# Performance work log

Measured on AMD Instinct MI355X. Metric: run time of the kernel, lower is better.

## Reference

```python
import jax, jax.numpy as jnp
import numpy as np

SCALE_POS = 2.0
SCALE_NEG = 50.0
THRESH = 0.7
MARGIN = 0.1
GAMMA = 0.3
EPS = 1e-5       # epsilon excluding self / near-duplicate positives
COS_EPS = 1e-8   # torch CosineSimilarity eps


def setup_inputs() -> dict:
    key = jax.random.key(0)
    k1, k2 = jax.random.split(key)
    B, D, C = 4096, 128, 256
    emb = jax.random.normal(k1, (B, D), dtype=jnp.float32)
    emb = emb / jnp.linalg.norm(emb, axis=1, keepdims=True)  # metric-learning embeddings are L2-normalized
    labels = jax.random.randint(k2, (B,), 0, C)
    return {"embeddings": emb, "labels": labels}


def reference(embeddings, labels):
    B = embeddings.shape[0]
    sim = embeddings @ embeddings.T                                   # [B,B]
    same = labels[:, None] == labels[None, :]
    pos_mask = same & (sim < 1.0 - EPS)
    neg_mask = ~same
    inf = jnp.inf
    min_pos = jnp.min(jnp.where(pos_mask, sim, inf), axis=1)          # [B] min(pos_pair_)
    max_neg = jnp.max(jnp.where(neg_mask, sim, -inf), axis=1)         # [B] max(neg_pair_)
    neg_keep = neg_mask & (sim + MARGIN > min_pos[:, None])           # mined negatives
    pos_keep = pos_mask & (sim - MARGIN < max_neg[:, None])           # mined positives
    valid = jnp.any(neg_keep, axis=1) & jnp.any(pos_keep, axis=1)
    # hardest positive index per anchor (argmin over kept positives; first-min tie-break like torch)
    j = jnp.argmin(jnp.where(pos_keep, sim, inf), axis=1)             # [B]
    d_p = embeddings[j] - embeddings                                  # f_p - f_a, [B,D]
    # dot[i,n] = (e_n - e_i) . d_p[i]
    dot = jnp.einsum('nd,id->in', embeddings, d_p) \
        - jnp.einsum('id,id->i', embeddings, d_p)[:, None]            # [B,B]
    sq = jnp.sum(embeddings * embeddings, axis=1)                     # [B]
    # ||e_n - e_i|| via Gram matrix; clamp avoids inf grad of sqrt at the diagonal (masked anyway)
    norm_n = jnp.sqrt(jnp.maximum(sq[None, :] + sq[:, None] - 2.0 * sim, 1e-12))
    norm_p = jnp.linalg.norm(d_p, axis=1)                             # [B] ||f_p - f_a||
    denom = jnp.maximum(norm_n, COS_EPS) * jnp.maximum(norm_p, COS_EPS)[:, None]
    reg = GAMMA * dot / denom                                         # [B,B] gamma * cos(f_n-f_a, f_p-f_a)
    pos_terms = jnp.where(pos_keep, jnp.exp(-SCALE_POS * (sim - THRESH)), 0.0)
    neg_terms = jnp.where(neg_keep, jnp.exp(SCALE_NEG * (sim - THRESH - reg)), 0.0)
    pos_loss = jnp.log1p(jnp.sum(pos_terms, axis=1)) / SCALE_POS
    neg_loss = jnp.log1p(jnp.sum(neg_terms, axis=1)) / SCALE_NEG
    row_loss = jnp.where(valid, pos_loss + neg_loss, 0.0)
    return jnp.sum(row_loss) / B
```

## Files before the change

### kernel.cpp

```cpp
#include <hip/hip_runtime.h>
#include <math.h>

#define NB 4096

#define SCALE_POS 2.0f
#define SCALE_NEG 50.0f
#define THRESH    0.7f
#define MARGIN    0.1f
#define GAMMA     0.3f
#define EPS_SELF  1e-5f

typedef __attribute__((ext_vector_type(8))) short s16x8;
typedef __attribute__((ext_vector_type(16))) float f32x16;
typedef unsigned long long u64;
typedef unsigned int u32;
typedef unsigned char u8;

__device__ __forceinline__ short f2bf(float x) {
  u32 u = __float_as_uint(x);
  return (short)((u + 0x7FFFu + ((u >> 16) & 1u)) >> 16);
}
__device__ __forceinline__ float bf2f(short h) {
  return __uint_as_float(((u32)(unsigned short)h) << 16);
}
__device__ __forceinline__ u32 mono16(u32 h) {
  return (h & 0x8000u) ? (h ^ 0xFFFFu) : (h | 0x8000u);
}
__device__ __forceinline__ float unmono16(u32 m) {
  u32 h = (m & 0x8000u) ? (m & 0x7FFFu) : (~m & 0xFFFFu);
  return bf2f((short)h);
}
__device__ __forceinline__ int Lmap(int p) {
  return (p & ~63) + 2 * (p & 31) + ((p >> 5) & 1);
}
__device__ __forceinline__ int Linv(int c) {
  return (c & ~63) + ((c & 1) << 5) + ((c >> 1) & 31);
}

__global__ __launch_bounds__(256) void k1_convert(
    const float* __restrict__ emb, const int* __restrict__ labels,
    short* __restrict__ F, u8* __restrict__ labu8) {
  int t = blockIdx.x * 256 + threadIdx.x;
  int T = t >> 9, s = (t >> 6) & 7, l = t & 63;
  int lrow = Lmap(T * 32 + (l & 31));
  int c4 = s * 4 + (l >> 5) * 2;
  const float4* e4 = (const float4*)emb;
  float4 v0 = e4[lrow * 32 + c4];
  float4 v1 = e4[lrow * 32 + c4 + 1];
  float xs[8] = {v0.x, v0.y, v0.z, v0.w, v1.x, v1.y, v1.z, v1.w};
  s16x8 h, lo;
#pragma unroll
  for (int e = 0; e < 8; ++e) {
    short hh = f2bf(xs[e]);
    h[e] = hh;
    lo[e] = f2bf(xs[e] - bf2f(hh));
  }
  ((s16x8*)F)[(T * 16 + s) * 64 + l] = h;
  ((s16x8*)F)[(T * 16 + 8 + s) * 64 + l] = lo;
  if (t < 1024) {
    int4 lb = ((const int4*)labels)[t];
    uchar4 p;
    p.x = (u8)lb.x; p.y = (u8)lb.y; p.z = (u8)lb.z; p.w = (u8)lb.w;
    ((uchar4*)labu8)[t] = p;
  }
}

__global__ __launch_bounds__(256, 4) void k2_pass1(
    const short* __restrict__ F, short* __restrict__ simh) {
  int tid = threadIdx.x, w = tid >> 6, l = tid & 63;
  int lo5 = l & 31, hi = l >> 5;
  int mt0 = blockIdx.y * 4 + (w >> 1) * 2;
  int nt0 = blockIdx.x * 4 + (w & 1) * 2;
  const s16x8* F8 = (const s16x8*)F;

  f32x16 acc[2][2] = {};
#pragma unroll 1
  for (int s = 0; s < 8; ++s) {
    s16x8 ah[2], al[2], bh[2], bl[2];
#pragma unroll
    for (int t = 0; t < 2; ++t) {
      int ia = ((mt0 + t) * 16 + s) * 64 + l;
      int ib = ((nt0 + t) * 16 + s) * 64 + l;
      ah[t] = F8[ia]; al[t] = F8[ia + 512];
      bh[t] = F8[ib]; bl[t] = F8[ib + 512];
    }
#pragma unroll
    for (int ti = 0; ti < 2; ++ti)
#pragma unroll
      for (int tj = 0; tj < 2; ++tj) {
        acc[ti][tj] = __builtin_amdgcn_mfma_f32_32x32x16_bf16(ah[ti], bh[tj], acc[ti][tj], 0, 0, 0);
        acc[ti][tj] = __builtin_amdgcn_mfma_f32_32x32x16_bf16(ah[ti], bl[tj], acc[ti][tj], 0, 0, 0);
        acc[ti][tj] = __builtin_amdgcn_mfma_f32_32x32x16_bf16(al[ti], bh[tj], acc[ti][tj], 0, 0, 0);
      }
  }

  u32* sim32 = (u32*)simh;
  int cg = nt0 >> 1;
#pragma unroll
  for (int ti = 0; ti < 2; ++ti)
#pragma unroll
    for (int q = 0; q < 4; ++q)
#pragma unroll
      for (int rr = 0; rr < 4; ++rr) {
        int reg = q * 4 + rr;
        int m = (mt0 + ti) * 32 + q * 8 + hi * 4 + rr;
        u32 pv = ((u32)(unsigned short)f2bf(acc[ti][1][reg]) << 16) |
                 (u32)(unsigned short)f2bf(acc[ti][0][reg]);
        sim32[(size_t)m * (NB / 2) + cg * 32 + lo5] = pv;
      }
}

__global__ __launch_bounds__(256) void k4_row(
    const short* __restrict__ simh, const u8* __restrict__ labu8,
    float* __restrict__ rowloss) {
  int w = threadIdx.x >> 6, l = threadIdx.x & 63;
  int r = w >> 1;
  int h = w & 1;
  int i = blockIdx.x * 2 + r;
  int lm = (int)labu8[Lmap(i)];
  const s16x8* sI = (const s16x8*)(simh + (size_t)i * NB);
  const u64* L8 = (const u64*)labu8;
  int cbase = h * 256;

  s16x8 a[4];
  u64 lab[4];
#pragma unroll
  for (int ch = 0; ch < 4; ++ch) a[ch] = sI[cbase + ch * 64 + l];
#pragma unroll
  for (int ch = 0; ch < 4; ++ch) lab[ch] = L8[cbase + ch * 64 + l];

  u32 pk = 0xFFFFFFFFu;
  u32 nk = 0u;
  u32 posm = 0u;
#pragma unroll
  for (int ch = 0; ch < 4; ++ch) {
    int nb = (cbase + ch * 64 + l) * 8;
#pragma unroll
    for (int e = 0; e < 8; ++e) {
      u32 hb = (u32)(unsigned short)a[ch][e];
      u32 key = (mono16(hb) << 16) | (u32)(nb + e);
      int ln = (int)((lab[ch] >> (8 * e)) & 255u);
      if (ln == lm) {
        posm |= (1u << (ch * 8 + e));
        float s = bf2f((short)hb);
        if (s < 1.0f - EPS_SELF) pk = pk < key ? pk : key;
      } else {
        nk = nk > key ? nk : key;
      }
    }
  }
#pragma unroll
  for (int d = 1; d < 64; d <<= 1) {
    u32 po = __shfl_xor(pk, d, 64); pk = pk < po ? pk : po;
    u32 no = __shfl_xor(nk, d, 64); nk = nk > no ? nk : no;
  }
  __shared__ u32 spk[4], snk[4];
  if (l == 0) { spk[w] = pk; snk[w] = nk; }
  __syncthreads();
  u32 P0 = spk[r * 2], P1 = spk[r * 2 + 1];
  u32 N0 = snk[r * 2], N1 = snk[r * 2 + 1];
  u32 Pk = P0 < P1 ? P0 : P1;
  u32 Nk = N0 > N1 ? N0 : N1;
  float minpos = unmono16(Pk >> 16);
  float maxneg = unmono16(Nk >> 16);
  bool valid = (maxneg + MARGIN > minpos);
  int jp = valid ? Linv((int)(Pk & 0xFFFFu)) : i;
  float mp = minpos, mx = maxneg;
  float dpp = minpos - 1.0f;
  float inpp = rsqrtf(fmaxf(2.0f - 2.0f * minpos, 1e-12f));

  const s16x8* sJ = (const s16x8*)(simh + (size_t)jp * NB);
  s16x8 b[4];
#pragma unroll
  for (int ch = 0; ch < 4; ++ch) b[ch] = sJ[cbase + ch * 64 + l];

  float ps = 0.0f, ns = 0.0f;
#pragma unroll
  for (int ch = 0; ch < 4; ++ch) {
#pragma unroll
    for (int e = 0; e < 8; ++e) {
      float s = bf2f(a[ch][e]);
      if ((posm >> (ch * 8 + e)) & 1u) {
        if (s < 1.0f - EPS_SELF && s - MARGIN < mx)
          ps += __expf(-SCALE_POS * (s - THRESH));
      } else if (s + MARGIN > mp) {
        float sjv = bf2f(b[ch][e]);
        float inn = rsqrtf(fmaxf(2.0f - 2.0f * s, 1e-12f));
        float rg = GAMMA * (sjv - s - dpp) * inpp * inn;
        ns += __expf(SCALE_NEG * (s - THRESH - rg));
      }
    }
  }
#pragma unroll
  for (int d = 1; d < 64; d <<= 1) {
    ps += __shfl_xor(ps, d, 64);
    ns += __shfl_xor(ns, d, 64);
  }
  __shared__ float redp[4], redn[4];
  if (l == 0) { redp[w] = ps; redn[w] = ns; }
  __syncthreads();
  if (l == 0 && h == 0) {
    float tp = redp[r * 2] + redp[r * 2 + 1];
    float tn = redn[r * 2] + redn[r * 2 + 1];
    rowloss[i] = valid ? (log1pf(tp) * (1.0f / SCALE_POS) + log1pf(tn) * (1.0f / SCALE_NEG))
                       : 0.0f;
  }
}

__global__ __launch_bounds__(1024) void k5_final(
    const float* __restrict__ rowloss, float* __restrict__ out) {
  int tid = threadIdx.x;
  float local = 0.0f;
  for (int r = tid; r < NB; r += 1024) local += rowloss[r];
#pragma unroll
  for (int d = 1; d < 64; d <<= 1) local += __shfl_xor(local, d, 64);
  __shared__ float partial[16];
  if ((tid & 63) == 0) partial[tid >> 6] = local;
  __syncthreads();
  if (tid == 0) {
    float t = 0.0f;
#pragma unroll
    for (int q = 0; q < 16; ++q) t += partial[q];
    out[0] = t / (float)NB;
  }
}

extern "C" void kernel_launch(void* const* d_in, const int* in_sizes, int n_in,
                              void* d_out, int out_size, void* d_ws, size_t ws_size,
                              hipStream_t stream) {
  const float* emb = (const float*)d_in[0];
  const int* labels = (const int*)d_in[1];
  float* out = (float*)d_out;
  char* ws = (char*)d_ws;

  short* simh = (short*)ws;
  short* F = (short*)(ws + ((size_t)NB * NB * 2));
  char* base = ws + ((size_t)NB * NB * 2) + (2 << 20);
  float* rowloss = (float*)(base);
  u8* labu8 = (u8*)(base + 16384);

  hipLaunchKernelGGL(k1_convert, dim3(256), dim3(256), 0, stream,
                     emb, labels, F, labu8);
  hipLaunchKernelGGL(k2_pass1, dim3(NB / 128, NB / 128), dim3(256), 0, stream,
                     F, simh);
  hipLaunchKernelGGL(k4_row, dim3(NB / 2), dim3(256), 0, stream,
                     simh, labu8, rowloss);
  hipLaunchKernelGGL(k5_final, dim3(1), dim3(1024), 0, stream, rowloss, out);
}
```

Before: 52.61 us.

## Fuse min-positive/max-negative mining into GEMM epilogue with atomic keys

Moves the per-row hardest-positive and hardest-negative key reduction from the row kernel into the GEMM epilogue. Each thread reduces packed (similarity, index) keys over its tile's column slice and merges them with global atomicMin/atomicMax, relying on the similarity matrix being symmetric. The init kernel resets the key arrays. This removes the row kernel's first reduction phase (shuffles, shared-memory sync and mask building), at the cost of extra label loads, compares and atomics in the GEMM epilogue.

```diff
diff --git a/kernel.cpp b/kernel.cpp
--- a/kernel.cpp
+++ b/kernel.cpp
@@ -33,13 +33,11 @@
 __device__ __forceinline__ int Lmap(int p) {
   return (p & ~63) + 2 * (p & 31) + ((p >> 5) & 1);
 }
-__device__ __forceinline__ int Linv(int c) {
-  return (c & ~63) + ((c & 1) << 5) + ((c >> 1) & 31);
-}
 
 __global__ __launch_bounds__(256) void k1_convert(
     const float* __restrict__ emb, const int* __restrict__ labels,
-    short* __restrict__ F, u8* __restrict__ labu8) {
+    short* __restrict__ F, u8* __restrict__ labu8,
+    u32* __restrict__ minkey, u32* __restrict__ maxkey) {
   int t = blockIdx.x * 256 + threadIdx.x;
   int T = t >> 9, s = (t >> 6) & 7, l = t & 63;
   int lrow = Lmap(T * 32 + (l & 31));
@@ -63,10 +61,16 @@
     p.x = (u8)lb.x; p.y = (u8)lb.y; p.z = (u8)lb.z; p.w = (u8)lb.w;
     ((uchar4*)labu8)[t] = p;
   }
+  if (t < NB) {
+    minkey[t] = 0xFFFFFFFFu;
+    maxkey[t] = 0u;
+  }
 }
 
 __global__ __launch_bounds__(256, 4) void k2_pass1(
-    const short* __restrict__ F, short* __restrict__ simh) {
+    const short* __restrict__ F, const u8* __restrict__ labu8,
+    short* __restrict__ simh,
+    u32* __restrict__ minkey, u32* __restrict__ maxkey) {
   int tid = threadIdx.x, w = tid >> 6, l = tid & 63;
   int lo5 = l & 31, hi = l >> 5;
   int mt0 = blockIdx.y * 4 + (w >> 1) * 2;
@@ -96,6 +100,11 @@
 
   u32* sim32 = (u32*)simh;
   int cg = nt0 >> 1;
+  int c0 = cg * 64 + 2 * lo5;
+  int lmc0 = (int)labu8[c0], lmc1 = (int)labu8[c0 + 1];
+  u32 mn0 = 0xFFFFFFFFu, mn1 = 0xFFFFFFFFu;
+  u32 mx0 = 0u, mx1 = 0u;
+
 #pragma unroll
   for (int ti = 0; ti < 2; ++ti)
 #pragma unroll
@@ -104,75 +113,63 @@
       for (int rr = 0; rr < 4; ++rr) {
         int reg = q * 4 + rr;
         int m = (mt0 + ti) * 32 + q * 8 + hi * 4 + rr;
-        u32 pv = ((u32)(unsigned short)f2bf(acc[ti][1][reg]) << 16) |
-                 (u32)(unsigned short)f2bf(acc[ti][0][reg]);
-        sim32[(size_t)m * (NB / 2) + cg * 32 + lo5] = pv;
+        u32 h0 = (u32)(unsigned short)f2bf(acc[ti][0][reg]);
+        u32 h1 = (u32)(unsigned short)f2bf(acc[ti][1][reg]);
+        sim32[(size_t)m * (NB / 2) + cg * 32 + lo5] = (h1 << 16) | h0;
+        int L = (m & ~63) + 2 * (m & 31) + ((m >> 5) & 1);
+        int lr = (int)labu8[L];
+        u32 k0 = (mono16(h0) << 16) | (u32)m;
+        u32 k1 = (mono16(h1) << 16) | (u32)m;
+        if (lr == lmc0) {
+          if (bf2f((short)h0) < 1.0f - EPS_SELF) mn0 = mn0 < k0 ? mn0 : k0;
+        } else {
+          mx0 = mx0 > k0 ? mx0 : k0;
+        }
+        if (lr == lmc1) {
+          if (bf2f((short)h1) < 1.0f - EPS_SELF) mn1 = mn1 < k1 ? mn1 : k1;
+        } else {
+          mx1 = mx1 > k1 ? mx1 : k1;
+        }
       }
+
+  atomicMin(&minkey[c0], mn0);
+  atomicMax(&maxkey[c0], mx0);
+  atomicMin(&minkey[c0 + 1], mn1);
+  atomicMax(&maxkey[c0 + 1], mx1);
 }
 
 __global__ __launch_bounds__(256) void k4_row(
     const short* __restrict__ simh, const u8* __restrict__ labu8,
+    const u32* __restrict__ minkey, const u32* __restrict__ maxkey,
     float* __restrict__ rowloss) {
   int w = threadIdx.x >> 6, l = threadIdx.x & 63;
   int r = w >> 1;
   int h = w & 1;
   int i = blockIdx.x * 2 + r;
-  int lm = (int)labu8[Lmap(i)];
-  const s16x8* sI = (const s16x8*)(simh + (size_t)i * NB);
-  const u64* L8 = (const u64*)labu8;
-  int cbase = h * 256;
-
-  s16x8 a[4];
-  u64 lab[4];
-#pragma unroll
-  for (int ch = 0; ch < 4; ++ch) a[ch] = sI[cbase + ch * 64 + l];
-#pragma unroll
-  for (int ch = 0; ch < 4; ++ch) lab[ch] = L8[cbase + ch * 64 + l];
-
-  u32 pk = 0xFFFFFFFFu;
-  u32 nk = 0u;
-  u32 posm = 0u;
-#pragma unroll
-  for (int ch = 0; ch < 4; ++ch) {
-    int nb = (cbase + ch * 64 + l) * 8;
-#pragma unroll
-    for (int e = 0; e < 8; ++e) {
-      u32 hb = (u32)(unsigned short)a[ch][e];
-      u32 key = (mono16(hb) << 16) | (u32)(nb + e);
-      int ln = (int)((lab[ch] >> (8 * e)) & 255u);
-      if (ln == lm) {
-        posm |= (1u << (ch * 8 + e));
-        float s = bf2f((short)hb);
-        if (s < 1.0f - EPS_SELF) pk = pk < key ? pk : key;
-      } else {
-        nk = nk > key ? nk : key;
-      }
-    }
-  }
-#pragma unroll
-  for (int d = 1; d < 64; d <<= 1) {
-    u32 po = __shfl_xor(pk, d, 64); pk = pk < po ? pk : po;
-    u32 no = __shfl_xor(nk, d, 64); nk = nk > no ? nk : no;
-  }
-  __shared__ u32 spk[4], snk[4];
-  if (l == 0) { spk[w] = pk; snk[w] = nk; }
-  __syncthreads();
-  u32 P0 = spk[r * 2], P1 = spk[r * 2 + 1];
-  u32 N0 = snk[r * 2], N1 = snk[r * 2 + 1];
-  u32 Pk = P0 < P1 ? P0 : P1;
-  u32 Nk = N0 > N1 ? N0 : N1;
+  int L = Lmap(i);
+  u32 Pk = minkey[L], Nk = maxkey[L];
   float minpos = unmono16(Pk >> 16);
   float maxneg = unmono16(Nk >> 16);
   bool valid = (maxneg + MARGIN > minpos);
-  int jp = valid ? Linv((int)(Pk & 0xFFFFu)) : i;
+  int jp = valid ? (int)(Pk & 0xFFFFu) : i;
+  int lm = (int)labu8[L];
   float mp = minpos, mx = maxneg;
   float dpp = minpos - 1.0f;
   float inpp = rsqrtf(fmaxf(2.0f - 2.0f * minpos, 1e-12f));
 
+  const s16x8* sI = (const s16x8*)(simh + (size_t)i * NB);
   const s16x8* sJ = (const s16x8*)(simh + (size_t)jp * NB);
-  s16x8 b[4];
+  const u64* L8 = (const u64*)labu8;
+  int cbase = h * 256;
+
+  s16x8 a[4], b[4];
+  u64 lab[4];
+#pragma unroll
+  for (int ch = 0; ch < 4; ++ch) a[ch] = sI[cbase + ch * 64 + l];
 #pragma unroll
   for (int ch = 0; ch < 4; ++ch) b[ch] = sJ[cbase + ch * 64 + l];
+#pragma unroll
+  for (int ch = 0; ch < 4; ++ch) lab[ch] = L8[cbase + ch * 64 + l];
 
   float ps = 0.0f, ns = 0.0f;
 #pragma unroll
@@ -180,7 +177,8 @@
 #pragma unroll
     for (int e = 0; e < 8; ++e) {
       float s = bf2f(a[ch][e]);
-      if ((posm >> (ch * 8 + e)) & 1u) {
+      int ln = (int)((lab[ch] >> (8 * e)) & 255u);
+      if (ln == lm) {
         if (s < 1.0f - EPS_SELF && s - MARGIN < mx)
           ps += __expf(-SCALE_POS * (s - THRESH));
       } else if (s + MARGIN > mp) {
@@ -238,12 +236,14 @@
   char* base = ws + ((size_t)NB * NB * 2) + (2 << 20);
   float* rowloss = (float*)(base);
   u8* labu8 = (u8*)(base + 16384);
+  u32* minkey = (u32*)(base + 20480);
+  u32* maxkey = (u32*)(base + 36864);
 
   hipLaunchKernelGGL(k1_convert, dim3(256), dim3(256), 0, stream,
-                     emb, labels, F, labu8);
+                     emb, labels, F, labu8, minkey, maxkey);
   hipLaunchKernelGGL(k2_pass1, dim3(NB / 128, NB / 128), dim3(256), 0, stream,
-                     F, simh);
+                     F, labu8, simh, minkey, maxkey);
   hipLaunchKernelGGL(k4_row, dim3(NB / 2), dim3(256), 0, stream,
-                     simh, labu8, rowloss);
+                     simh, labu8, minkey, maxkey, rowloss);
   hipLaunchKernelGGL(k5_final, dim3(1), dim3(1024), 0, stream, rowloss, out);
 }
```

Result: slower. 59.30 us (+12.7%).
